# Kernel optimization log

Measured on AMD Instinct MI355X. Metric: run time of the kernel, lower is better.

## Reference

```python
import jax, jax.numpy as jnp
import numpy as np

B, M, N = 4, 2048, 2048
C, H, HD, L = 256, 4, 64, 9
THR = 0.1


def _rope(x, cos, sin):
    # x: (B,H,N,HD); cos/sin: (B,1,N,HD) with pair-interleaved values
    x1 = x[..., 0::2]
    x2 = x[..., 1::2]
    rot = jnp.stack([-x2, x1], axis=-1).reshape(x.shape)
    return x * cos + rot * sin


def _heads(x, b, n):
    return x.reshape(b, n, H, HD).transpose(0, 2, 1, 3)


def _merge(x, b, n):
    return x.transpose(0, 2, 1, 3).reshape(b, n, H * HD)


def _ffn(x, msg, W1, b1, g, beta, W2, b2):
    h = jnp.concatenate([x, msg], axis=-1) @ W1 + b1
    mu = h.mean(-1, keepdims=True)
    var = h.var(-1, keepdims=True)
    h = (h - mu) * jax.lax.rsqrt(var + 1e-5) * g + beta
    return jax.nn.gelu(h) @ W2 + b2


def _self_block(x, cos, sin, Wqkv, bqkv, Wo, bo, ff):
    b, n, _ = x.shape
    q, k, v = jnp.split(x @ Wqkv + bqkv, 3, axis=-1)
    q = _rope(_heads(q, b, n), cos, sin)
    k = _rope(_heads(k, b, n), cos, sin)
    v = _heads(v, b, n)
    attn = jax.nn.softmax(jnp.einsum('bhmd,bhnd->bhmn', q, k) / jnp.sqrt(jnp.float32(HD)), axis=-1)
    msg = _merge(jnp.einsum('bhmn,bhnd->bhmd', attn, v), b, n) @ Wo + bo
    return x + _ffn(x, msg, *ff)


def _cross_block(x0, x1, Wqk, bqk, Wv, bv, Wo, bo, ff):
    b, m, _ = x0.shape
    n = x1.shape[1]
    s = HD ** -0.25
    qk0 = _heads(x0 @ Wqk + bqk, b, m) * s
    qk1 = _heads(x1 @ Wqk + bqk, b, n) * s
    v0 = _heads(x0 @ Wv + bv, b, m)
    v1 = _heads(x1 @ Wv + bv, b, n)
    sim = jnp.einsum('bhmd,bhnd->bhmn', qk0, qk1)
    m0 = jnp.einsum('bhmn,bhnd->bhmd', jax.nn.softmax(sim, axis=3), v1)
    m1 = jnp.einsum('bhmn,bhmd->bhnd', jax.nn.softmax(sim, axis=2), v0)
    m0 = _merge(m0, b, m) @ Wo + bo
    m1 = _merge(m1, b, n) @ Wo + bo
    return x0 + _ffn(x0, m0, *ff), x1 + _ffn(x1, m1, *ff)


def _posenc(kpts, size, Wr):
    shift = size / 2.0
    scale = size.max() / 2.0
    knorm = (kpts - shift) / scale                      # (B,N,2)
    proj = knorm @ Wr                                   # (B,N,HD//2)
    cos = jnp.repeat(jnp.cos(proj), 2, axis=-1)[:, None, :, :]  # (B,1,N,HD)
    sin = jnp.repeat(jnp.sin(proj), 2, axis=-1)[:, None, :, :]
    return cos, sin


def setup_inputs() -> dict:
    key = jax.random.key(0)
    def nrm(i, shape, s=0.02):
        return (s * jax.random.normal(jax.random.fold_in(key, i), shape)).astype(jnp.float32)
    def uni(i, shape):
        return jax.random.uniform(jax.random.fold_in(key, i), shape, jnp.float32)
    wh = jnp.array([1024.0, 768.0], jnp.float32)
    return {
        'kpts0': uni(0, (B, M, 2)) * wh,
        'desc0': nrm(1, (B, M, C), 1.0),
        'kpts1': uni(2, (B, N, 2)) * wh,
        'desc1': nrm(3, (B, N, C), 1.0),
        'image_size': wh,
        'Wr': nrm(4, (2, HD // 2), 1.0),
        'saqkv_W': nrm(5, (L, C, 3 * C)),
        'saqkv_b': jnp.zeros((L, 3 * C), jnp.float32),
        'saout_W': nrm(6, (L, C, C)),
        'saout_b': jnp.zeros((L, C), jnp.float32),
        'saff_W1': nrm(7, (L, 2 * C, 2 * C)),
        'saff_b1': jnp.zeros((L, 2 * C), jnp.float32),
        'saff_g': jnp.ones((L, 2 * C), jnp.float32),
        'saff_beta': jnp.zeros((L, 2 * C), jnp.float32),
        'saff_W2': nrm(8, (L, 2 * C, C)),
        'saff_b2': jnp.zeros((L, C), jnp.float32),
        'caqk_W': nrm(9, (L, C, C)),
        'caqk_b': jnp.zeros((L, C), jnp.float32),
        'cav_W': nrm(10, (L, C, C)),
        'cav_b': jnp.zeros((L, C), jnp.float32),
        'caout_W': nrm(11, (L, C, C)),
        'caout_b': jnp.zeros((L, C), jnp.float32),
        'caff_W1': nrm(12, (L, 2 * C, 2 * C)),
        'caff_b1': jnp.zeros((L, 2 * C), jnp.float32),
        'caff_g': jnp.ones((L, 2 * C), jnp.float32),
        'caff_beta': jnp.zeros((L, 2 * C), jnp.float32),
        'caff_W2': nrm(13, (L, 2 * C, C)),
        'caff_b2': jnp.zeros((L, C), jnp.float32),
        'fproj_W': nrm(14, (C, C)),
        'fproj_b': jnp.zeros((C,), jnp.float32),
        'match_w': nrm(15, (C,)),
        'match_b': jnp.zeros((), jnp.float32),
    }


def reference(kpts0, desc0, kpts1, desc1, image_size, Wr,
              saqkv_W, saqkv_b, saout_W, saout_b,
              saff_W1, saff_b1, saff_g, saff_beta, saff_W2, saff_b2,
              caqk_W, caqk_b, cav_W, cav_b, caout_W, caout_b,
              caff_W1, caff_b1, caff_g, caff_beta, caff_W2, caff_b2,
              fproj_W, fproj_b, match_w, match_b):
    cos0, sin0 = _posenc(kpts0, image_size, Wr)
    cos1, sin1 = _posenc(kpts1, image_size, Wr)
    d0, d1 = desc0, desc1
    for i in range(L):
        ffs = (saff_W1[i], saff_b1[i], saff_g[i], saff_beta[i], saff_W2[i], saff_b2[i])
        d0 = _self_block(d0, cos0, sin0, saqkv_W[i], saqkv_b[i], saout_W[i], saout_b[i], ffs)
        d1 = _self_block(d1, cos1, sin1, saqkv_W[i], saqkv_b[i], saout_W[i], saout_b[i], ffs)
        ffc = (caff_W1[i], caff_b1[i], caff_g[i], caff_beta[i], caff_W2[i], caff_b2[i])
        d0, d1 = _cross_block(d0, d1, caqk_W[i], caqk_b[i], cav_W[i], cav_b[i], caout_W[i], caout_b[i], ffc)
    # sigmoid log-double-softmax assignment
    scale = C ** 0.25
    md0 = (d0 @ fproj_W + fproj_b) / scale
    md1 = (d1 @ fproj_W + fproj_b) / scale
    sim = jnp.einsum('bmd,bnd->bmn', md0, md1)
    z0 = d0 @ match_w + match_b                         # (B,M)
    z1 = d1 @ match_w + match_b                         # (B,N)
    inner = (jax.nn.log_softmax(sim, axis=2) + jax.nn.log_softmax(sim, axis=1)
             + jax.nn.log_sigmoid(z0)[:, :, None] + jax.nn.log_sigmoid(z1)[:, None, :])
    scores = jnp.zeros((B, M + 1, N + 1), sim.dtype)
    scores = scores.at[:, :M, :N].set(inner)
    scores = scores.at[:, :M, N].set(jax.nn.log_sigmoid(-z0))
    scores = scores.at[:, M, :N].set(jax.nn.log_sigmoid(-z1))
    # filter_matches: mutual nearest neighbor + threshold
    valid = scores[:, :-1, :-1]
    max0 = valid.max(axis=2)
    argmax0 = valid.argmax(axis=2)
    argmax1 = valid.argmax(axis=1)
    idx0 = jnp.arange(M)[None, :]
    idx1 = jnp.arange(N)[None, :]
    mutual0 = idx0 == jnp.take_along_axis(argmax1, argmax0, axis=1)
    mutual1 = idx1 == jnp.take_along_axis(argmax0, argmax1, axis=1)
    mscores0 = jnp.where(mutual0, jnp.exp(max0), 0.0)
    mscores1 = jnp.where(mutual1, jnp.take_along_axis(mscores0, argmax1, axis=1), 0.0)
    valid0 = mutual0 & (mscores0 > THR)
    valid1 = mutual1 & jnp.take_along_axis(valid0, argmax1, axis=1)
    m0 = jnp.where(valid0, argmax0, -1)
    m1 = jnp.where(valid1, argmax1, -1)
    return m0, m1, mscores0, mscores1, scores
```

## Files before the change

### kernel.cpp

```cpp
#include <hip/hip_runtime.h>
#include <hip/hip_bf16.h>
#include <cmath>

#define DEVI __device__ __forceinline__

constexpr int B_   = 4;
constexpr int M_   = 2048;
constexpr int C_   = 256;
constexpr int H_   = 4;
constexpr int HD_  = 64;
constexpr int L_   = 9;
constexpr int TOK_ = B_ * M_;
constexpr int C2_  = 2 * C_;
constexpr int C3_  = 3 * C_;
constexpr int NS_  = 2049;

typedef __attribute__((ext_vector_type(8))) short s16x8;
typedef __attribute__((ext_vector_type(4))) float f32x4;
typedef __attribute__((ext_vector_type(4))) unsigned short u16x4;

DEVI float logsig_f(float x) {
  if (x >= 0.0f) return -log1pf(__expf(-x));
  return x - log1pf(__expf(x));
}

DEVI float gelu_tanh(float x) {
  float x3 = x * x * x;
  float t = 0.7978845608028654f * (x + 0.044715f * x3);
  return x / (1.0f + __expf(-2.0f * t));
}

DEVI unsigned short f2bf(float x) {
  unsigned u = __float_as_uint(x);
  u += 0x7fffu + ((u >> 16) & 1u);
  return (unsigned short)(u >> 16);
}
DEVI float bf2f(unsigned short h) { return __uint_as_float((unsigned)h << 16); }

__global__ void posenc_kernel(const float* __restrict__ kpts, const float* __restrict__ wh,
                              const float* __restrict__ Wr, float* __restrict__ cc,
                              float* __restrict__ sc) {
  int idx = blockIdx.x * blockDim.x + threadIdx.x;
  if (idx >= B_ * M_ * 32) return;
  int j  = idx & 31;
  int bm = idx >> 5;
  float w = wh[0], h = wh[1];
  float smax = fmaxf(w, h) * 0.5f;
  float kx = (kpts[bm * 2 + 0] - w * 0.5f) / smax;
  float ky = (kpts[bm * 2 + 1] - h * 0.5f) / smax;
  float p = kx * Wr[j] + ky * Wr[32 + j];
  cc[bm * 32 + j] = cosf(p);
  sc[bm * 32 + j] = sinf(p);
}

__global__ void wconv_kernel(const float* __restrict__ W, unsigned short* __restrict__ Th,
                             unsigned short* __restrict__ Tl, int kbits, int N) {
  int idx = blockIdx.x * 256 + threadIdx.x;
  int k = idx & ((1 << kbits) - 1);
  int n = idx >> kbits;
  float x = W[(size_t)k * N + n];
  unsigned short h = f2bf(x);
  Th[idx] = h;
  Tl[idx] = f2bf(x - bf2f(h));
}

__global__ void wconv_layer_kernel(const float* __restrict__ qkv, const float* __restrict__ saout,
                                   const float* __restrict__ sw1, const float* __restrict__ sw2,
                                   const float* __restrict__ cqk, const float* __restrict__ cv,
                                   const float* __restrict__ cout_, const float* __restrict__ cw1,
                                   const float* __restrict__ cw2,
                                   unsigned short* __restrict__ Th, unsigned short* __restrict__ Tl) {
  int idx = blockIdx.x * 256 + threadIdx.x;
  const float* src; int kbits, N, rel;
  if      (idx <  196608) { src = qkv;   kbits = 8; N = 768; rel = idx; }
  else if (idx <  262144) { src = saout; kbits = 8; N = 256; rel = idx -  196608; }
  else if (idx <  524288) { src = sw1;   kbits = 9; N = 512; rel = idx -  262144; }
  else if (idx <  655360) { src = sw2;   kbits = 9; N = 256; rel = idx -  524288; }
  else if (idx <  720896) { src = cqk;   kbits = 8; N = 256; rel = idx -  655360; }
  else if (idx <  786432) { src = cv;    kbits = 8; N = 256; rel = idx -  720896; }
  else if (idx <  851968) { src = cout_; kbits = 8; N = 256; rel = idx -  786432; }
  else if (idx < 1114112) { src = cw1;   kbits = 9; N = 512; rel = idx -  851968; }
  else                    { src = cw2;   kbits = 9; N = 256; rel = idx - 1114112; }
  int k = rel & ((1 << kbits) - 1), n = rel >> kbits;
  float x = src[(size_t)k * N + n];
  unsigned short h = f2bf(x);
  Th[idx] = h;
  Tl[idx] = f2bf(x - bf2f(h));
}

__global__ void split_kernel(const float* __restrict__ src, unsigned short* __restrict__ h,
                             unsigned short* __restrict__ l) {
  int idx = blockIdx.x * 256 + threadIdx.x;
  float x = src[idx];
  unsigned short hb = f2bf(x);
  h[idx] = hb;
  l[idx] = f2bf(x - bf2f(hb));
}

__global__ __launch_bounds__(256) void prep_ropeqk_kernel(
    const float* __restrict__ S, const float* __restrict__ cc, const float* __restrict__ sc,
    unsigned short* __restrict__ Qh, unsigned short* __restrict__ Ql,
    unsigned short* __restrict__ Kh, unsigned short* __restrict__ Kl) {
  int idx = blockIdx.x * 256 + threadIdx.x;
  int j = idx & 31;
  int h = (idx >> 5) & 3;
  int tok = idx >> 7;
  int m = tok & 2047, b = tok >> 11;
  const float* row = S + (size_t)tok * 768 + h * 64 + 2 * j;
  float c = cc[(size_t)tok * 32 + j];
  float s = sc[(size_t)tok * 32 + j];
  float2 q = *(const float2*)row;
  float2 k = *(const float2*)(row + 256);
  float qx = q.x * c - q.y * s, qy = q.y * c + q.x * s;
  float kx = k.x * c - k.y * s, ky = k.y * c + k.x * s;
  size_t o = ((size_t)(b * 4 + h) * 2048 + m) * 64 + 2 * j;
  unsigned short q0 = f2bf(qx), q1 = f2bf(qy);
  ushort2 t;
  t.x = q0; t.y = q1;                       *(ushort2*)&Qh[o] = t;
  t.x = f2bf(qx - bf2f(q0)); t.y = f2bf(qy - bf2f(q1)); *(ushort2*)&Ql[o] = t;
  unsigned short k0 = f2bf(kx), k1 = f2bf(ky);
  t.x = k0; t.y = k1;                       *(ushort2*)&Kh[o] = t;
  t.x = f2bf(kx - bf2f(k0)); t.y = f2bf(ky - bf2f(k1)); *(ushort2*)&Kl[o] = t;
}

__global__ __launch_bounds__(256) void prep_vt_kernel(
    const float* __restrict__ S, int ld, int vcol,
    unsigned short* __restrict__ Vth, unsigned short* __restrict__ Vtl) {
  int idx = blockIdx.x * 256 + threadIdx.x;
  int mq = idx & 511; int m0 = mq << 2;
  int d = (idx >> 9) & 63;
  int bh = idx >> 15;
  int b = bh >> 2, h = bh & 3;
  const float* base = S + ((size_t)(b * 2048) + m0) * ld + vcol + h * 64 + d;
  u16x4 hv, lv;
#pragma unroll
  for (int i = 0; i < 4; i++) {
    float x = base[(size_t)i * ld];
    unsigned short hb = f2bf(x);
    hv[i] = hb;
    lv[i] = f2bf(x - bf2f(hb));
  }
  size_t o = ((size_t)bh * 64 + d) * 2048 + m0;
  *(u16x4*)&Vth[o] = hv;
  *(u16x4*)&Vtl[o] = lv;
}

__global__ __launch_bounds__(256, 3) void mgemm_kernel(
    const unsigned short* __restrict__ A1h, const unsigned short* __restrict__ A1l,
    const unsigned short* __restrict__ A2h, const unsigned short* __restrict__ A2l,
    int lda, int kSplit,
    const unsigned short* __restrict__ WTh, const unsigned short* __restrict__ WTl,
    const float* __restrict__ bias, const float* __restrict__ res,
    float* __restrict__ outf, int ldo,
    unsigned short* __restrict__ outh, unsigned short* __restrict__ outl, int nsplit,
    unsigned short* __restrict__ tvh, unsigned short* __restrict__ tvl,
    int K, float oscale) {
  __shared__ alignas(16) unsigned short Ash[128 * 64];
  __shared__ alignas(16) unsigned short Asl[128 * 64];
  __shared__ alignas(16) unsigned short Bsh[64 * 64];
  __shared__ alignas(16) unsigned short Bsl[64 * 64];
  int tid = threadIdx.x;
  int rowBase = blockIdx.y << 7;
  int colBase = blockIdx.x << 6;
  int lr = tid & 15, lg = (tid >> 4) & 3;
  int wid = tid >> 6, wm = wid >> 1, wn = wid & 1;
  int sw = (lr & 7) << 3;
  f32x4 acc[4][2] = {};

  for (int k0 = 0; k0 < K; k0 += 64) {
    const unsigned short *Ah, *Al;
    int kloc;
    if (k0 < kSplit) { Ah = A1h; Al = A1l; kloc = k0; }
    else             { Ah = A2h; Al = A2l; kloc = k0 - kSplit; }
    __syncthreads();
#pragma unroll
    for (int i = 0; i < 8; i++) {
      int idx = tid + (i << 8);
      int r = idx >> 4;
      int kc = (idx & 15) << 2;
      size_t g = (size_t)(rowBase + r) * lda + kloc + kc;
      u16x4 hv = *(const u16x4*)&Ah[g];
      u16x4 lv = *(const u16x4*)&Al[g];
      int col = kc ^ ((r & 7) << 3);
      *(u16x4*)&Ash[r * 64 + col] = hv;
      *(u16x4*)&Asl[r * 64 + col] = lv;
    }
#pragma unroll
    for (int i = 0; i < 4; i++) {
      int idx = tid + (i << 8);
      int rn = idx >> 4;
      int kc = (idx & 15) << 2;
      size_t g = (size_t)(colBase + rn) * K + k0 + kc;
      u16x4 hv = *(const u16x4*)&WTh[g];
      u16x4 lv = *(const u16x4*)&WTl[g];
      int col = kc ^ ((rn & 7) << 3);
      *(u16x4*)&Bsh[rn * 64 + col] = hv;
      *(u16x4*)&Bsl[rn * 64 + col] = lv;
    }
    __syncthreads();
#pragma unroll
    for (int c = 0; c < 2; c++) {
      int kcol = (c << 5) + (lg << 3);
      s16x8 ah[4], al[4], bh[2], bl[2];
#pragma unroll
      for (int mi = 0; mi < 4; mi++) {
        int off = (wm * 64 + mi * 16 + lr) * 64 + (kcol ^ sw);
        ah[mi] = *(const s16x8*)&Ash[off];
        al[mi] = *(const s16x8*)&Asl[off];
      }
#pragma unroll
      for (int ni = 0; ni < 2; ni++) {
        int off = (wn * 32 + ni * 16 + lr) * 64 + (kcol ^ sw);
        bh[ni] = *(const s16x8*)&Bsh[off];
        bl[ni] = *(const s16x8*)&Bsl[off];
      }
#pragma unroll
      for (int mi = 0; mi < 4; mi++)
#pragma unroll
        for (int ni = 0; ni < 2; ni++) {
          f32x4 t = acc[mi][ni];
          t = __builtin_amdgcn_mfma_f32_16x16x32_bf16(ah[mi], bl[ni], t, 0, 0, 0);
          t = __builtin_amdgcn_mfma_f32_16x16x32_bf16(al[mi], bh[ni], t, 0, 0, 0);
          t = __builtin_amdgcn_mfma_f32_16x16x32_bf16(ah[mi], bh[ni], t, 0, 0, 0);
          acc[mi][ni] = t;
        }
    }
  }
#pragma unroll
  for (int mi = 0; mi < 4; mi++) {
    int row0 = rowBase + wm * 64 + mi * 16 + lg * 4;
#pragma unroll
    for (int ni = 0; ni < 2; ni++) {
      int col = colBase + wn * 32 + ni * 16 + lr;
      float bc = bias ? bias[col] : 0.0f;
      float vj[4];
      size_t of0 = (size_t)row0 * ldo + col;
#pragma unroll
      for (int j = 0; j < 4; j++) {
        float v = (acc[mi][ni][j] + bc) * oscale;
        if (res) v += res[of0 + (size_t)j * ldo];
        vj[j] = v;
      }
      if (outf) {
#pragma unroll
        for (int j = 0; j < 4; j++) outf[of0 + (size_t)j * ldo] = vj[j];
      }
      bool plain = outh && (col < nsplit);
      if (plain) {
        size_t o0 = (size_t)row0 * 256 + col;
#pragma unroll
        for (int j = 0; j < 4; j++) {
          unsigned short hb = f2bf(vj[j]);
          outh[o0 + (size_t)j * 256] = hb;
          outl[o0 + (size_t)j * 256] = f2bf(vj[j] - bf2f(hb));
        }
      } else if (tvh) {
        int cc2 = outh ? (col - nsplit) : col;
        int hh = cc2 >> 6, d = cc2 & 63;
        int bb = row0 >> 11, m0 = row0 & 2047;
        u16x4 hv, lv;
#pragma unroll
        for (int j = 0; j < 4; j++) {
          unsigned short hb = f2bf(vj[j]);
          hv[j] = hb;
          lv[j] = f2bf(vj[j] - bf2f(hb));
        }
        size_t tvo = ((size_t)(bb * 4 + hh) * 64 + d) * 2048 + m0;
        *(u16x4*)&tvh[tvo] = hv;
        *(u16x4*)&tvl[tvo] = lv;
      }
    }
  }
}

__global__ __launch_bounds__(256, 2) void flashm2_kernel(
    const unsigned short* __restrict__ Qh, const unsigned short* __restrict__ Ql, int ldq, int hq,
    const unsigned short* __restrict__ Kh, const unsigned short* __restrict__ Kl, int ldk, int hk,
    const unsigned short* __restrict__ Vth, const unsigned short* __restrict__ Vtl,
    unsigned short* __restrict__ Oh, unsigned short* __restrict__ Ol, float scale) {
  __shared__ alignas(16) unsigned short Ksh[64 * 64];
  __shared__ alignas(16) unsigned short Ksl[64 * 64];
  __shared__ alignas(16) unsigned short Vsh[64 * 64];
  __shared__ alignas(16) unsigned short Vsl[64 * 64];
  __shared__ alignas(16) unsigned short Ph[64 * 64];
  __shared__ alignas(16) unsigned short Pl[64 * 64];
  int bh = blockIdx.y;
  int b = bh >> 2, h = bh & 3;
  int mBase = blockIdx.x * 64;
  size_t qbase = (size_t)b * (M_ * C_) + (size_t)h * hq;
  size_t kbase = (size_t)b * (M_ * C_) + (size_t)h * hk;
  size_t vbase = (size_t)bh * (64 * 2048);
  int tid = threadIdx.x;
  int lane = tid & 63, w = tid >> 6;
  int lr = lane & 15, lg = lane >> 4;

  s16x8 qh[2], ql[2];
  {
    int m = mBase + w * 16 + lr;
#pragma unroll
    for (int c = 0; c < 2; c++) {
      size_t g = qbase + (size_t)m * ldq + c * 32 + lg * 8;
      qh[c] = *(const s16x8*)&Qh[g];
      ql[c] = *(const s16x8*)&Ql[g];
    }
  }

  float m_run[4], l_run[4];
  f32x4 oacc[4];
#pragma unroll
  for (int j = 0; j < 4; j++) { m_run[j] = -INFINITY; l_run[j] = 0.0f; }
#pragma unroll
  for (int g = 0; g < 4; g++) oacc[g] = (f32x4){0.f, 0.f, 0.f, 0.f};

  for (int t0 = 0; t0 < M_; t0 += 64) {
    __syncthreads();
#pragma unroll
    for (int i = 0; i < 4; i++) {
      int idx = tid + (i << 8);
      int key = idx >> 4;
      int d0 = (idx & 15) << 2;
      size_t g = kbase + (size_t)(t0 + key) * ldk + d0;
      int cswz = d0 ^ ((key & 7) << 3);
      *(u16x4*)&Ksh[key * 64 + cswz] = *(const u16x4*)&Kh[g];
      *(u16x4*)&Ksl[key * 64 + cswz] = *(const u16x4*)&Kl[g];
      int d = idx >> 4;
      int kc = (idx & 15) << 2;
      size_t gv = vbase + (size_t)d * 2048 + t0 + kc;
      int kk = kc ^ (((d ^ (d >> 2)) & 7) << 3);
      *(u16x4*)&Vsh[d * 64 + kk] = *(const u16x4*)&Vth[gv];
      *(u16x4*)&Vsl[d * 64 + kk] = *(const u16x4*)&Vtl[gv];
    }
    __syncthreads();

    f32x4 sacc[4];
#pragma unroll
    for (int f = 0; f < 4; f++) sacc[f] = (f32x4){0.f, 0.f, 0.f, 0.f};
#pragma unroll
    for (int f = 0; f < 4; f++) {
#pragma unroll
      for (int c = 0; c < 2; c++) {
        int key = f * 16 + lr;
        int kb = c * 32 + lg * 8;
        int off = key * 64 + (kb ^ ((key & 7) << 3));
        s16x8 kh = *(const s16x8*)&Ksh[off];
        s16x8 kl = *(const s16x8*)&Ksl[off];
        f32x4 t = sacc[f];
        t = __builtin_amdgcn_mfma_f32_16x16x32_bf16(qh[c], kl, t, 0, 0, 0);
        t = __builtin_amdgcn_mfma_f32_16x16x32_bf16(ql[c], kh, t, 0, 0, 0);
        t = __builtin_amdgcn_mfma_f32_16x16x32_bf16(qh[c], kh, t, 0, 0, 0);
        sacc[f] = t;
      }
    }
#pragma unroll
    for (int f = 0; f < 4; f++)
#pragma unroll
      for (int j = 0; j < 4; j++) sacc[f][j] *= scale;

    float mnew[4], alpha[4], lsum[4];
#pragma unroll
    for (int j = 0; j < 4; j++) {
      float v = fmaxf(fmaxf(sacc[0][j], sacc[1][j]), fmaxf(sacc[2][j], sacc[3][j]));
      v = fmaxf(v, __shfl_xor(v, 1));
      v = fmaxf(v, __shfl_xor(v, 2));
      v = fmaxf(v, __shfl_xor(v, 4));
      v = fmaxf(v, __shfl_xor(v, 8));
      mnew[j] = fmaxf(m_run[j], v);
      alpha[j] = __expf(m_run[j] - mnew[j]);
      lsum[j] = 0.0f;
    }
#pragma unroll
    for (int f = 0; f < 4; f++) {
#pragma unroll
      for (int j = 0; j < 4; j++) {
        float p = __expf(sacc[f][j] - mnew[j]);
// ... 194 lines not shown
  if (lane == 0) { max_out[row] = best; am_out[row] = bi; }
}

__global__ void colamax1_kernel(const float* __restrict__ sco, float* __restrict__ pv,
                                int* __restrict__ pi) {
  int col = blockIdx.x * 256 + threadIdx.x;
  int rc = blockIdx.y, b = blockIdx.z;
  const float* base = sco + (size_t)b * NS_ * NS_ + col;
  float best = -INFINITY; int bi = 0;
  for (int r = rc * 256; r < rc * 256 + 256; r++) {
    float v = base[(size_t)r * NS_];
    if (v > best) { best = v; bi = r; }
  }
  size_t o = ((size_t)b * 8 + rc) * 2048 + col;
  pv[o] = best; pi[o] = bi;
}

__global__ void colamax2_kernel(const float* __restrict__ pv, const int* __restrict__ pi,
                                int* __restrict__ am1) {
  int i = blockIdx.x * 256 + threadIdx.x;
  int b = i >> 11, col = i & 2047;
  float best = -INFINITY; int bi = 0;
  for (int rc = 0; rc < 8; rc++) {
    size_t o = ((size_t)b * 8 + rc) * 2048 + col;
    float v = pv[o];
    if (v > best) { best = v; bi = pi[o]; }
  }
  am1[i] = bi;
}

__global__ void edge_kernel(const float* __restrict__ lsn0, const float* __restrict__ lsn1,
                            float* __restrict__ sco) {
  int i = blockIdx.x * blockDim.x + threadIdx.x;
  if (i >= B_ * M_) return;
  int b = i >> 11, t = i & 2047;
  sco[((size_t)b * NS_ + t) * NS_ + 2048] = lsn0[i];
  sco[((size_t)b * NS_ + 2048) * NS_ + t] = lsn1[i];
  if (t == 0) sco[((size_t)b * NS_ + 2048) * NS_ + 2048] = 0.0f;
}

__global__ void match0ws_kernel(const int* __restrict__ am0, const int* __restrict__ am1,
                                const float* __restrict__ max0, float* __restrict__ ms0f,
                                int* __restrict__ val0) {
  int i = blockIdx.x * blockDim.x + threadIdx.x;
  if (i >= B_ * M_) return;
  int b = i >> 11, m = i & 2047;
  int a0 = am0[i];
  bool mutual = (am1[b * M_ + a0] == m);
  float ms = mutual ? __expf(max0[i]) : 0.0f;
  ms0f[i] = ms;
  val0[i] = (mutual && ms > 0.1f) ? 1 : 0;
}

__global__ void finalout_kernel(const int* __restrict__ am0, const int* __restrict__ am1,
                                const float* __restrict__ ms0f, const int* __restrict__ val0,
                                float* __restrict__ out) {
  int i = blockIdx.x * blockDim.x + threadIdx.x;
  if (i >= B_ * M_) return;
  int b = i >> 11, t = i & 2047;
  int a0 = am0[i];
  bool mut0 = (am1[b * M_ + a0] == t);
  float ms0 = ms0f[i];
  bool v0 = mut0 && (ms0 > 0.1f);
  out[i] = v0 ? (float)a0 : -1.0f;
  out[2 * B_ * M_ + i] = ms0;
  int a1 = am1[i];
  bool mut1 = (am0[b * M_ + a1] == t);
  float ms1 = mut1 ? ms0f[b * M_ + a1] : 0.0f;
  bool v1 = mut1 && (val0[b * M_ + a1] != 0);
  out[B_ * M_ + i] = v1 ? (float)a1 : -1.0f;
  out[3 * B_ * M_ + i] = ms1;
}

constexpr size_t WOFF_QKV   = 0;
constexpr size_t WOFF_SAOUT = 196608;
constexpr size_t WOFF_SAW1  = 262144;
constexpr size_t WOFF_SAW2  = 524288;
constexpr size_t WOFF_CAQK  = 655360;
constexpr size_t WOFF_CAOUT = 786432;
constexpr size_t WOFF_CAW1  = 851968;
constexpr size_t WOFF_CAW2  = 1114112;
constexpr size_t WELEMS_    = 1245184;

constexpr size_t PLN   = (size_t)TOK_ * C_;
constexpr size_t OXS0  = 2 * WELEMS_;
constexpr size_t OXS1  = OXS0 + 2 * PLN;
constexpr size_t OBA   = OXS1 + 2 * PLN;
constexpr size_t OBB   = OBA + 2 * PLN;
constexpr size_t OBC   = OBB + 2 * PLN;
constexpr size_t OBD   = OBC + 2 * PLN;
constexpr size_t OBE   = OBD + 2 * PLN;

extern "C" void kernel_launch(void* const* d_in, const int* in_sizes, int n_in,
                              void* d_out, int out_size, void* d_ws, size_t ws_size,
                              hipStream_t stream) {
  const float* kpts0      = (const float*)d_in[0];
  const float* desc0      = (const float*)d_in[1];
  const float* kpts1      = (const float*)d_in[2];
  const float* desc1      = (const float*)d_in[3];
  const float* image_size = (const float*)d_in[4];
  const float* Wr         = (const float*)d_in[5];
  const float* saqkv_W    = (const float*)d_in[6];
  const float* saqkv_b    = (const float*)d_in[7];
  const float* saout_W    = (const float*)d_in[8];
  const float* saout_b    = (const float*)d_in[9];
  const float* saff_W1    = (const float*)d_in[10];
  const float* saff_b1    = (const float*)d_in[11];
  const float* saff_g     = (const float*)d_in[12];
  const float* saff_beta  = (const float*)d_in[13];
  const float* saff_W2    = (const float*)d_in[14];
  const float* saff_b2    = (const float*)d_in[15];
  const float* caqk_W     = (const float*)d_in[16];
  const float* caqk_b     = (const float*)d_in[17];
  const float* cav_W      = (const float*)d_in[18];
  const float* cav_b      = (const float*)d_in[19];
  const float* caout_W    = (const float*)d_in[20];
  const float* caout_b    = (const float*)d_in[21];
  const float* caff_W1    = (const float*)d_in[22];
  const float* caff_b1    = (const float*)d_in[23];
  const float* caff_g     = (const float*)d_in[24];
  const float* caff_beta  = (const float*)d_in[25];
  const float* caff_W2    = (const float*)d_in[26];
  const float* caff_b2    = (const float*)d_in[27];
  const float* fproj_W    = (const float*)d_in[28];
  const float* fproj_b    = (const float*)d_in[29];
  const float* match_w    = (const float*)d_in[30];
  const float* match_b    = (const float*)d_in[31];

  float* ofp = (float*)d_out;
  float* SCO = ofp + 4 * B_ * M_;
  unsigned short* SCu = (unsigned short*)SCO;

  constexpr size_t N = (size_t)TOK_ * C_;
  constexpr size_t Qc = (size_t)B_ * M_ * 32;
  float* Wp  = (float*)d_ws;
  float* D0  = Wp;
  float* D1  = D0 + N;
  float* CC0 = D1 + N;
  float* SC0 = CC0 + Qc;
  float* CC1 = SC0 + Qc;
  float* SC1 = CC1 + Qc;
  float* S0  = SC1 + Qc;
  float* S1  = S0 + N;
  float* S2  = S1 + N;
  float* S3  = S2 + N;
  float* S4  = S3 + N;
  (void)S4;

  unsigned short* WTH = SCu;
  unsigned short* WTL = SCu + WELEMS_;

  float* LS0  = S2;
  float* LSN0 = LS0 + 8192;
  float* LS1  = LSN0 + 8192;
  float* LSN1 = LS1 + 8192;
  float* RT   = LSN1 + 8192;
  float* CT   = RT + 8192;
  float* MAX0 = CT + 8192;
  float* MS0F = MAX0 + 8192;
  int*   AM0  = (int*)(MS0F + 8192);
  int*   AM1  = AM0 + 8192;
  int*   VAL0 = AM1 + 8192;
  float* CB   = (float*)(VAL0 + 8192);
  float* PM = S3;
  float* PL = PM + 65536;
  float* PV = PL + 65536;
  int*   PI = (int*)(PV + 65536);
  unsigned short* MD0u = (unsigned short*)S0;
  unsigned short* MD1u = (unsigned short*)S1;

  auto Hp = [&](size_t off) { return SCu + off; };
  auto Lp = [&](size_t off) { return SCu + off + PLN; };

  auto mgemm = [&](const unsigned short* a1h, const unsigned short* a1l,
                   const unsigned short* a2h, const unsigned short* a2l,
                   int lda, int kSplit, const unsigned short* wth, const unsigned short* wtl,
                   const float* bias, const float* res, float* outf, int ldo,
                   unsigned short* outh, unsigned short* outl, int nsplit,
                   unsigned short* tvh, unsigned short* tvl,
                   int K, int Ncols, int Mrows, float osc) {
    mgemm_kernel<<<dim3(Ncols >> 6, Mrows >> 7), 256, 0, stream>>>(
        a1h, a1l, a2h, a2l, lda, kSplit, wth, wtl,
        bias, res, outf, ldo, outh, outl, nsplit, tvh, tvl, K, osc);
  };

  auto ffn = [&](float* X, unsigned short* xsh, unsigned short* xsl,
                 unsigned short* msgh, unsigned short* msgl,
                 size_t offW1, const float* b1, const float* g, const float* be,
                 size_t offW2, const float* b2) {
    mgemm(xsh, xsl, msgh, msgl, C_, C_, WTH + offW1, WTL + offW1,
          b1, nullptr, S0, C2_, nullptr, nullptr, 0, nullptr, nullptr, C2_, C2_, TOK_, 1.0f);
    ln_gelu_kernel<<<TOK_, 256, 0, stream>>>(S0, g, be, Hp(OBC), Hp(OBD));
    mgemm(Hp(OBC), Hp(OBD), Hp(OBC), Hp(OBD), C2_, C2_, WTH + offW2, WTL + offW2,
          b2, X, X, C_, xsh, xsl, C_, nullptr, nullptr, C2_, C_, TOK_, 1.0f);
  };

  auto self_block = [&](float* X, unsigned short* xsh, unsigned short* xsl,
                        const float* cc, const float* sc, int l) {
    const float* bqkv = saqkv_b + (size_t)l * C3_;
    const float* bo   = saout_b + (size_t)l * C_;
    mgemm(xsh, xsl, xsh, xsl, C_, C_, WTH + WOFF_QKV, WTL + WOFF_QKV,
          bqkv, nullptr, S0, C3_, nullptr, nullptr, 0, nullptr, nullptr, C_, C3_, TOK_, 1.0f);
    prep_ropeqk_kernel<<<4096, 256, 0, stream>>>(S0, cc, sc, Hp(OBA), Lp(OBA), Hp(OBB), Lp(OBB));
    prep_vt_kernel<<<2048, 256, 0, stream>>>(S0, C3_, C2_, Hp(OBC), Lp(OBC));
    flashm2_kernel<<<dim3(M_ / 64, B_ * H_), 256, 0, stream>>>(
        Hp(OBA), Lp(OBA), 64, 2048 * 64, Hp(OBB), Lp(OBB), 64, 2048 * 64,
        Hp(OBC), Lp(OBC), Hp(OBE), Lp(OBE), 0.125f);
    mgemm(Hp(OBE), Lp(OBE), Hp(OBE), Lp(OBE), C_, C_, WTH + WOFF_SAOUT, WTL + WOFF_SAOUT,
          bo, nullptr, nullptr, C_, Hp(OBA), Lp(OBA), C_, nullptr, nullptr, C_, C_, TOK_, 1.0f);
    ffn(X, xsh, xsl, Hp(OBA), Lp(OBA),
        WOFF_SAW1, saff_b1 + (size_t)l * C2_,
        saff_g + (size_t)l * C2_, saff_beta + (size_t)l * C2_,
        WOFF_SAW2, saff_b2 + (size_t)l * C_);
  };

  auto cross_block = [&](int l) {
    const float* bo  = caout_b + (size_t)l * C_;
    const float* b1  = caff_b1 + (size_t)l * C2_;
    const float* g   = caff_g + (size_t)l * C2_;
    const float* be  = caff_beta + (size_t)l * C2_;
    const float* b2  = caff_b2 + (size_t)l * C_;
    hipMemcpyAsync(CB, caqk_b + (size_t)l * C_, C_ * sizeof(float),
                   hipMemcpyDeviceToDevice, stream);
    hipMemcpyAsync(CB + C_, cav_b + (size_t)l * C_, C_ * sizeof(float),
                   hipMemcpyDeviceToDevice, stream);
    mgemm(Hp(OXS0), Lp(OXS0), Hp(OXS0), Lp(OXS0), C_, C_, WTH + WOFF_CAQK, WTL + WOFF_CAQK,
          CB, nullptr, nullptr, C_, Hp(OBA), Lp(OBA), C_, Hp(OBC), Lp(OBC), C_, C2_, TOK_, 1.0f);
    mgemm(Hp(OXS1), Lp(OXS1), Hp(OXS1), Lp(OXS1), C_, C_, WTH + WOFF_CAQK, WTL + WOFF_CAQK,
          CB, nullptr, nullptr, C_, Hp(OBB), Lp(OBB), C_, Hp(OBD), Lp(OBD), C_, C2_, TOK_, 1.0f);
    flashm2_kernel<<<dim3(M_ / 64, B_ * H_), 256, 0, stream>>>(
        Hp(OBA), Lp(OBA), C_, 64, Hp(OBB), Lp(OBB), C_, 64,
        Hp(OBD), Lp(OBD), Hp(OBE), Lp(OBE), 0.125f);
    flashm2_kernel<<<dim3(M_ / 64, B_ * H_), 256, 0, stream>>>(
        Hp(OBB), Lp(OBB), C_, 64, Hp(OBA), Lp(OBA), C_, 64,
        Hp(OBC), Lp(OBC), Hp(OBD), Lp(OBD), 0.125f);
    mgemm(Hp(OBE), Lp(OBE), Hp(OBE), Lp(OBE), C_, C_, WTH + WOFF_CAOUT, WTL + WOFF_CAOUT,
          bo, nullptr, nullptr, C_, Hp(OBA), Lp(OBA), C_, nullptr, nullptr, C_, C_, TOK_, 1.0f);
    mgemm(Hp(OBD), Lp(OBD), Hp(OBD), Lp(OBD), C_, C_, WTH + WOFF_CAOUT, WTL + WOFF_CAOUT,
          bo, nullptr, nullptr, C_, Hp(OBB), Lp(OBB), C_, nullptr, nullptr, C_, C_, TOK_, 1.0f);
    ffn(D0, Hp(OXS0), Lp(OXS0), Hp(OBA), Lp(OBA), WOFF_CAW1, b1, g, be, WOFF_CAW2, b2);
    ffn(D1, Hp(OXS1), Lp(OXS1), Hp(OBB), Lp(OBB), WOFF_CAW1, b1, g, be, WOFF_CAW2, b2);
  };

  hipMemcpyAsync(D0, desc0, N * sizeof(float), hipMemcpyDeviceToDevice, stream);
  hipMemcpyAsync(D1, desc1, N * sizeof(float), hipMemcpyDeviceToDevice, stream);
  split_kernel<<<PLN / 256, 256, 0, stream>>>(desc0, Hp(OXS0), Lp(OXS0));
  split_kernel<<<PLN / 256, 256, 0, stream>>>(desc1, Hp(OXS1), Lp(OXS1));
  posenc_kernel<<<(B_ * M_ * 32 + 255) / 256, 256, 0, stream>>>(kpts0, image_size, Wr, CC0, SC0);
  posenc_kernel<<<(B_ * M_ * 32 + 255) / 256, 256, 0, stream>>>(kpts1, image_size, Wr, CC1, SC1);

  for (int l = 0; l < L_; l++) {
    wconv_layer_kernel<<<WELEMS_ / 256, 256, 0, stream>>>(
        saqkv_W + (size_t)l * C_ * C3_, saout_W + (size_t)l * C_ * C_,
        saff_W1 + (size_t)l * C2_ * C2_, saff_W2 + (size_t)l * C2_ * C_,
        caqk_W + (size_t)l * C_ * C_, cav_W + (size_t)l * C_ * C_,
        caout_W + (size_t)l * C_ * C_, caff_W1 + (size_t)l * C2_ * C2_,
        caff_W2 + (size_t)l * C2_ * C_, WTH, WTL);
    self_block(D0, Hp(OXS0), Lp(OXS0), CC0, SC0, l);
    self_block(D1, Hp(OXS1), Lp(OXS1), CC1, SC1, l);
    cross_block(l);
  }

  wconv_kernel<<<(C_ << 8) >> 8, 256, 0, stream>>>(fproj_W, WTH, WTL, 8, C_);
  mgemm(Hp(OXS0), Lp(OXS0), Hp(OXS0), Lp(OXS0), C_, C_, WTH, WTL,
        fproj_b, nullptr, nullptr, C_, MD0u, MD0u + PLN, C_, nullptr, nullptr,
        C_, C_, TOK_, 0.25f);
  mgemm(Hp(OXS1), Lp(OXS1), Hp(OXS1), Lp(OXS1), C_, C_, WTH, WTL,
        fproj_b, nullptr, nullptr, C_, MD1u, MD1u + PLN, C_, nullptr, nullptr,
        C_, C_, TOK_, 0.25f);
  z_kernel<<<2048, 256, 0, stream>>>(D0, match_w, match_b, LS0, LSN0);
  z_kernel<<<2048, 256, 0, stream>>>(D1, match_w, match_b, LS1, LSN1);
  for (int b = 0; b < B_; b++) {
    size_t ao = (size_t)b * M_ * C_;
    mgemm(MD0u + ao, MD0u + PLN + ao, MD0u + ao, MD0u + PLN + ao, C_, C_,
          MD1u + ao, MD1u + PLN + ao, nullptr, nullptr,
          SCO + (size_t)b * NS_ * NS_, NS_, nullptr, nullptr, 0, nullptr, nullptr,
          C_, M_, M_, 2.0f);
  }
  edge_kernel<<<32, 256, 0, stream>>>(LSN0, LSN1, SCO);
  lse_row_kernel<<<2048, 256, 0, stream>>>(SCO, LS0, RT);
  colred1_kernel<<<dim3(8, 8, 4), 256, 0, stream>>>(SCO, PM, PL);
  colred2_kernel<<<32, 256, 0, stream>>>(PM, PL, LS1, CT);
  upd_rowargmax_kernel<<<2048, 256, 0, stream>>>(RT, CT, SCO, MAX0, AM0);
  colamax1_kernel<<<dim3(8, 8, 4), 256, 0, stream>>>(SCO, PV, PI);
  colamax2_kernel<<<32, 256, 0, stream>>>(PV, PI, AM1);
  match0ws_kernel<<<32, 256, 0, stream>>>(AM0, AM1, MAX0, MS0F, VAL0);
  finalout_kernel<<<32, 256, 0, stream>>>(AM0, AM1, MS0F, VAL0, ofp);

  (void)in_sizes; (void)n_in; (void)out_size; (void)ws_size;
}
```

Measured before the change: 7.933 ms.

## Fuse RoPE/V-transpose into QKV GEMM epilogue and batch both images per launch

Moves the RoPE rotation and the bf16 hi/lo split of Q/K, plus the transposed V write, into the QKV GEMM epilogue, using a lane shuffle to fetch the paired element. This removes the fp32 QKV round trip and two prep kernels. It also lays out both images' activations contiguously so the out-projections, FFNs, cross QK/V projection and final projection each run as one launch over 2x tokens. Cross-attention biases are packed once up front instead of by per-layer memcpys. The cost is a more complex GEMM epilogue with scattered 2-byte stores and a reworked buffer-aliasing scheme that has to stay correct.

```diff
diff --git a/kernel.cpp b/kernel.cpp
--- a/kernel.cpp
+++ b/kernel.cpp
@@ -88,6 +88,14 @@
   Tl[idx] = f2bf(x - bf2f(h));
 }
 
+__global__ void cbias_kernel(const float* __restrict__ qkb, const float* __restrict__ vb,
+                             float* __restrict__ cb) {
+  int i = blockIdx.x * 256 + threadIdx.x;
+  if (i >= L_ * 512) return;
+  int l = i >> 9, c = i & 511;
+  cb[i] = (c < 256) ? qkb[l * 256 + c] : vb[l * 256 + (c - 256)];
+}
+
 __global__ void split_kernel(const float* __restrict__ src, unsigned short* __restrict__ h,
                              unsigned short* __restrict__ l) {
   int idx = blockIdx.x * 256 + threadIdx.x;
@@ -95,54 +103,6 @@
   unsigned short hb = f2bf(x);
   h[idx] = hb;
   l[idx] = f2bf(x - bf2f(hb));
-}
-
-__global__ __launch_bounds__(256) void prep_ropeqk_kernel(
-    const float* __restrict__ S, const float* __restrict__ cc, const float* __restrict__ sc,
-    unsigned short* __restrict__ Qh, unsigned short* __restrict__ Ql,
-    unsigned short* __restrict__ Kh, unsigned short* __restrict__ Kl) {
-  int idx = blockIdx.x * 256 + threadIdx.x;
-  int j = idx & 31;
-  int h = (idx >> 5) & 3;
-  int tok = idx >> 7;
-  int m = tok & 2047, b = tok >> 11;
-  const float* row = S + (size_t)tok * 768 + h * 64 + 2 * j;
-  float c = cc[(size_t)tok * 32 + j];
-  float s = sc[(size_t)tok * 32 + j];
-  float2 q = *(const float2*)row;
-  float2 k = *(const float2*)(row + 256);
-  float qx = q.x * c - q.y * s, qy = q.y * c + q.x * s;
-  float kx = k.x * c - k.y * s, ky = k.y * c + k.x * s;
-  size_t o = ((size_t)(b * 4 + h) * 2048 + m) * 64 + 2 * j;
-  unsigned short q0 = f2bf(qx), q1 = f2bf(qy);
-  ushort2 t;
-  t.x = q0; t.y = q1;                       *(ushort2*)&Qh[o] = t;
-  t.x = f2bf(qx - bf2f(q0)); t.y = f2bf(qy - bf2f(q1)); *(ushort2*)&Ql[o] = t;
-  unsigned short k0 = f2bf(kx), k1 = f2bf(ky);
-  t.x = k0; t.y = k1;                       *(ushort2*)&Kh[o] = t;
-  t.x = f2bf(kx - bf2f(k0)); t.y = f2bf(ky - bf2f(k1)); *(ushort2*)&Kl[o] = t;
-}
-
-__global__ __launch_bounds__(256) void prep_vt_kernel(
-    const float* __restrict__ S, int ld, int vcol,
-    unsigned short* __restrict__ Vth, unsigned short* __restrict__ Vtl) {
-  int idx = blockIdx.x * 256 + threadIdx.x;
-  int mq = idx & 511; int m0 = mq << 2;
-  int d = (idx >> 9) & 63;
-  int bh = idx >> 15;
-  int b = bh >> 2, h = bh & 3;
-  const float* base = S + ((size_t)(b * 2048) + m0) * ld + vcol + h * 64 + d;
-  u16x4 hv, lv;
-#pragma unroll
-  for (int i = 0; i < 4; i++) {
-    float x = base[(size_t)i * ld];
-    unsigned short hb = f2bf(x);
-    hv[i] = hb;
-    lv[i] = f2bf(x - bf2f(hb));
-  }
-  size_t o = ((size_t)bh * 64 + d) * 2048 + m0;
-  *(u16x4*)&Vth[o] = hv;
-  *(u16x4*)&Vtl[o] = lv;
 }
 
 __global__ __launch_bounds__(256, 3) void mgemm_kernel(
@@ -154,6 +114,9 @@
     float* __restrict__ outf, int ldo,
     unsigned short* __restrict__ outh, unsigned short* __restrict__ outl, int nsplit,
     unsigned short* __restrict__ tvh, unsigned short* __restrict__ tvl,
+    const float* __restrict__ ccp, const float* __restrict__ scp,
+    unsigned short* __restrict__ qph, unsigned short* __restrict__ qpl,
+    unsigned short* __restrict__ kph, unsigned short* __restrict__ kpl,
     int K, float oscale) {
   __shared__ alignas(16) unsigned short Ash[128 * 64];
   __shared__ alignas(16) unsigned short Asl[128 * 64];
@@ -241,33 +204,73 @@
         if (res) v += res[of0 + (size_t)j * ldo];
         vj[j] = v;
       }
-      if (outf) {
-#pragma unroll
-        for (int j = 0; j < 4; j++) outf[of0 + (size_t)j * ldo] = vj[j];
-      }
-      bool plain = outh && (col < nsplit);
-      if (plain) {
-        size_t o0 = (size_t)row0 * 256 + col;
-#pragma unroll
-        for (int j = 0; j < 4; j++) {
-          unsigned short hb = f2bf(vj[j]);
-          outh[o0 + (size_t)j * 256] = hb;
-          outl[o0 + (size_t)j * 256] = f2bf(vj[j] - bf2f(hb));
+      if (ccp) {
+        if (col < 512) {
+          float pv[4];
+#pragma unroll
+          for (int j = 0; j < 4; j++) pv[j] = __shfl_xor(vj[j], 1);
+          int d = col & 63;
+          int hh = (col >> 6) & 3;
+          int ji = (d >> 1) & 31;
+          bool isK = col >= 256;
+          unsigned short* dh = isK ? kph : qph;
+          unsigned short* dl = isK ? kpl : qpl;
+          int bb = row0 >> 11;
+#pragma unroll
+          for (int j = 0; j < 4; j++) {
+            int tok = row0 + j;
+            float c = ccp[(size_t)tok * 32 + ji];
+            float s = scp[(size_t)tok * 32 + ji];
+            float r = (col & 1) ? (vj[j] * c + pv[j] * s)
+                                : (vj[j] * c - pv[j] * s);
+            size_t o = ((size_t)(bb * 4 + hh) * 2048 + (tok & 2047)) * 64 + d;
+            unsigned short hb = f2bf(r);
+            dh[o] = hb;
+            dl[o] = f2bf(r - bf2f(hb));
+          }
+        } else {
+          int cc2 = col - 512;
+          int hh = cc2 >> 6, d = cc2 & 63;
+          int bb = row0 >> 11, mv = row0 & 2047;
+          u16x4 hv, lv;
+#pragma unroll
+          for (int j = 0; j < 4; j++) {
+            unsigned short hb = f2bf(vj[j]);
+            hv[j] = hb; lv[j] = f2bf(vj[j] - bf2f(hb));
+          }
+          size_t tvo = ((size_t)(bb * 4 + hh) * 64 + d) * 2048 + mv;
+          *(u16x4*)&tvh[tvo] = hv;
+          *(u16x4*)&tvl[tvo] = lv;
         }
-      } else if (tvh) {
-        int cc2 = outh ? (col - nsplit) : col;
-        int hh = cc2 >> 6, d = cc2 & 63;
-        int bb = row0 >> 11, m0 = row0 & 2047;
-        u16x4 hv, lv;
-#pragma unroll
-        for (int j = 0; j < 4; j++) {
-          unsigned short hb = f2bf(vj[j]);
-          hv[j] = hb;
-          lv[j] = f2bf(vj[j] - bf2f(hb));
+      } else {
+        if (outf) {
+#pragma unroll
+          for (int j = 0; j < 4; j++) outf[of0 + (size_t)j * ldo] = vj[j];
         }
-        size_t tvo = ((size_t)(bb * 4 + hh) * 64 + d) * 2048 + m0;
-        *(u16x4*)&tvh[tvo] = hv;
-        *(u16x4*)&tvl[tvo] = lv;
+        bool plain = outh && (col < nsplit);
+        if (plain) {
+          size_t o0 = (size_t)row0 * 256 + col;
+#pragma unroll
+          for (int j = 0; j < 4; j++) {
+            unsigned short hb = f2bf(vj[j]);
+            outh[o0 + (size_t)j * 256] = hb;
+            outl[o0 + (size_t)j * 256] = f2bf(vj[j] - bf2f(hb));
+          }
+        } else if (tvh) {
+          int cc2 = outh ? (col - nsplit) : col;
+          int hh = cc2 >> 6, d = cc2 & 63;
+          int bb = row0 >> 11, mv = row0 & 2047;
+          u16x4 hv, lv;
+#pragma unroll
+          for (int j = 0; j < 4; j++) {
+            unsigned short hb = f2bf(vj[j]);
+            hv[j] = hb;
+            lv[j] = f2bf(vj[j] - bf2f(hb));
+          }
+          size_t tvo = ((size_t)(bb * 4 + hh) * 64 + d) * 2048 + mv;
+          *(u16x4*)&tvh[tvo] = hv;
+          *(u16x4*)&tvl[tvo] = lv;
+        }
       }
     }
   }
@@ -276,7 +279,7 @@
 __global__ __launch_bounds__(256, 2) void flashm2_kernel(
     const unsigned short* __restrict__ Qh, const unsigned short* __restrict__ Ql, int ldq, int hq,
     const unsigned short* __restrict__ Kh, const unsigned short* __restrict__ Kl, int ldk, int hk,
-    const unsigned short* __restrict__ Vth, const unsigned short* __restrict__ Vtl,
+    const unsigned short* __restrict__ Vth, const unsigned short* __restrict__ Vtl, int voff,
     unsigned short* __restrict__ Oh, unsigned short* __restrict__ Ol, float scale) {
   __shared__ alignas(16) unsigned short Ksh[64 * 64];
   __shared__ alignas(16) unsigned short Ksl[64 * 64];
@@ -289,7 +292,7 @@
   int mBase = blockIdx.x * 64;
   size_t qbase = (size_t)b * (M_ * C_) + (size_t)h * hq;
   size_t kbase = (size_t)b * (M_ * C_) + (size_t)h * hk;
-  size_t vbase = (size_t)bh * (64 * 2048);
+  size_t vbase = (size_t)(voff + bh) * (64 * 2048);
   int tid = threadIdx.x;
   int lane = tid & 63, w = tid >> 6;
   int lr = lane & 15, lg = lane >> 4;
@@ -650,14 +653,10 @@
 constexpr size_t WOFF_CAW2  = 1114112;
 constexpr size_t WELEMS_    = 1245184;
 
-constexpr size_t PLN   = (size_t)TOK_ * C_;
-constexpr size_t OXS0  = 2 * WELEMS_;
-constexpr size_t OXS1  = OXS0 + 2 * PLN;
-constexpr size_t OBA   = OXS1 + 2 * PLN;
-constexpr size_t OBB   = OBA + 2 * PLN;
-constexpr size_t OBC   = OBB + 2 * PLN;
-constexpr size_t OBD   = OBC + 2 * PLN;
-constexpr size_t OBE   = OBD + 2 * PLN;
+constexpr size_t PLN  = (size_t)TOK_ * C_;
+constexpr size_t XHO  = 2 * WELEMS_;
+constexpr size_t XLO  = XHO + 2 * PLN;
+constexpr size_t POOL = XLO + 2 * PLN;
 
 extern "C" void kernel_launch(void* const* d_in, const int* in_sizes, int n_in,
                               void* d_out, int out_size, void* d_ws, size_t ws_size,
@@ -713,10 +712,12 @@
   float* S2  = S1 + N;
   float* S3  = S2 + N;
   float* S4  = S3 + N;
-  (void)S4;
 
   unsigned short* WTH = SCu;
   unsigned short* WTL = SCu + WELEMS_;
+  unsigned short* XH  = SCu + XHO;
+  unsigned short* XL  = SCu + XLO;
+  auto Pu = [&](int k) { return SCu + POOL + (size_t)k * PLN; };
 
   float* LS0  = S2;
   float* LSN0 = LS0 + 8192;
@@ -729,93 +730,46 @@
   int*   AM0  = (int*)(MS0F + 8192);
   int*   AM1  = AM0 + 8192;
   int*   VAL0 = AM1 + 8192;
-  float* CB   = (float*)(VAL0 + 8192);
   float* PM = S3;
   float* PL = PM + 65536;
   float* PV = PL + 65536;
   int*   PI = (int*)(PV + 65536);
-  unsigned short* MD0u = (unsigned short*)S0;
-  unsigned short* MD1u = (unsigned short*)S1;
-
-  auto Hp = [&](size_t off) { return SCu + off; };
-  auto Lp = [&](size_t off) { return SCu + off + PLN; };
-
-  auto mgemm = [&](const unsigned short* a1h, const unsigned short* a1l,
-                   const unsigned short* a2h, const unsigned short* a2l,
-                   int lda, int kSplit, const unsigned short* wth, const unsigned short* wtl,
-                   const float* bias, const float* res, float* outf, int ldo,
-                   unsigned short* outh, unsigned short* outl, int nsplit,
-                   unsigned short* tvh, unsigned short* tvl,
-                   int K, int Ncols, int Mrows, float osc) {
+  float* CB = S4;
+  unsigned short* MDu = (unsigned short*)S0;
+
+  auto mg = [&](const unsigned short* a1h, const unsigned short* a1l,
+                const unsigned short* a2h, const unsigned short* a2l,
+                int lda, int kSplit, const unsigned short* wth, const unsigned short* wtl,
+                const float* bias, const float* res, float* outf, int ldo,
+                unsigned short* outh, unsigned short* outl, int nsplit,
+                unsigned short* tvh, unsigned short* tvl,
+                const float* ccp, const float* scp,
+                unsigned short* qph, unsigned short* qpl,
+                unsigned short* kph, unsigned short* kpl,
+                int K, int Ncols, int Mrows, float osc) {
     mgemm_kernel<<<dim3(Ncols >> 6, Mrows >> 7), 256, 0, stream>>>(
-        a1h, a1l, a2h, a2l, lda, kSplit, wth, wtl,
-        bias, res, outf, ldo, outh, outl, nsplit, tvh, tvl, K, osc);
+        a1h, a1l, a2h, a2l, lda, kSplit, wth, wtl, bias, res, outf, ldo,
+        outh, outl, nsplit, tvh, tvl, ccp, scp, qph, qpl, kph, kpl, K, osc);
   };
 
-  auto ffn = [&](float* X, unsigned short* xsh, unsigned short* xsl,
-                 unsigned short* msgh, unsigned short* msgl,
-                 size_t offW1, const float* b1, const float* g, const float* be,
-                 size_t offW2, const float* b2) {
-    mgemm(xsh, xsl, msgh, msgl, C_, C_, WTH + offW1, WTL + offW1,
-          b1, nullptr, S0, C2_, nullptr, nullptr, 0, nullptr, nullptr, C2_, C2_, TOK_, 1.0f);
-    ln_gelu_kernel<<<TOK_, 256, 0, stream>>>(S0, g, be, Hp(OBC), Hp(OBD));
-    mgemm(Hp(OBC), Hp(OBD), Hp(OBC), Hp(OBD), C2_, C2_, WTH + offW2, WTL + offW2,
-          b2, X, X, C_, xsh, xsl, C_, nullptr, nullptr, C2_, C_, TOK_, 1.0f);
-  };
-
-  auto self_block = [&](float* X, unsigned short* xsh, unsigned short* xsl,
-                        const float* cc, const float* sc, int l) {
-    const float* bqkv = saqkv_b + (size_t)l * C3_;
-    const float* bo   = saout_b + (size_t)l * C_;
-    mgemm(xsh, xsl, xsh, xsl, C_, C_, WTH + WOFF_QKV, WTL + WOFF_QKV,
-          bqkv, nullptr, S0, C3_, nullptr, nullptr, 0, nullptr, nullptr, C_, C3_, TOK_, 1.0f);
-    prep_ropeqk_kernel<<<4096, 256, 0, stream>>>(S0, cc, sc, Hp(OBA), Lp(OBA), Hp(OBB), Lp(OBB));
-    prep_vt_kernel<<<2048, 256, 0, stream>>>(S0, C3_, C2_, Hp(OBC), Lp(OBC));
-    flashm2_kernel<<<dim3(M_ / 64, B_ * H_), 256, 0, stream>>>(
-        Hp(OBA), Lp(OBA), 64, 2048 * 64, Hp(OBB), Lp(OBB), 64, 2048 * 64,
-        Hp(OBC), Lp(OBC), Hp(OBE), Lp(OBE), 0.125f);
-    mgemm(Hp(OBE), Lp(OBE), Hp(OBE), Lp(OBE), C_, C_, WTH + WOFF_SAOUT, WTL + WOFF_SAOUT,
-          bo, nullptr, nullptr, C_, Hp(OBA), Lp(OBA), C_, nullptr, nullptr, C_, C_, TOK_, 1.0f);
-    ffn(X, xsh, xsl, Hp(OBA), Lp(OBA),
-        WOFF_SAW1, saff_b1 + (size_t)l * C2_,
-        saff_g + (size_t)l * C2_, saff_beta + (size_t)l * C2_,
-        WOFF_SAW2, saff_b2 + (size_t)l * C_);
-  };
-
-  auto cross_block = [&](int l) {
-    const float* bo  = caout_b + (size_t)l * C_;
-    const float* b1  = caff_b1 + (size_t)l * C2_;
-    const float* g   = caff_g + (size_t)l * C2_;
-    const float* be  = caff_beta + (size_t)l * C2_;
-    const float* b2  = caff_b2 + (size_t)l * C_;
-    hipMemcpyAsync(CB, caqk_b + (size_t)l * C_, C_ * sizeof(float),
-                   hipMemcpyDeviceToDevice, stream);
-    hipMemcpyAsync(CB + C_, cav_b + (size_t)l * C_, C_ * sizeof(float),
-                   hipMemcpyDeviceToDevice, stream);
-    mgemm(Hp(OXS0), Lp(OXS0), Hp(OXS0), Lp(OXS0), C_, C_, WTH + WOFF_CAQK, WTL + WOFF_CAQK,
-          CB, nullptr, nullptr, C_, Hp(OBA), Lp(OBA), C_, Hp(OBC), Lp(OBC), C_, C2_, TOK_, 1.0f);
-    mgemm(Hp(OXS1), Lp(OXS1), Hp(OXS1), Lp(OXS1), C_, C_, WTH + WOFF_CAQK, WTL + WOFF_CAQK,
-          CB, nullptr, nullptr, C_, Hp(OBB), Lp(OBB), C_, Hp(OBD), Lp(OBD), C_, C2_, TOK_, 1.0f);
-    flashm2_kernel<<<dim3(M_ / 64, B_ * H_), 256, 0, stream>>>(
-        Hp(OBA), Lp(OBA), C_, 64, Hp(OBB), Lp(OBB), C_, 64,
-        Hp(OBD), Lp(OBD), Hp(OBE), Lp(OBE), 0.125f);
-    flashm2_kernel<<<dim3(M_ / 64, B_ * H_), 256, 0, stream>>>(
-        Hp(OBB), Lp(OBB), C_, 64, Hp(OBA), Lp(OBA), C_, 64,
-        Hp(OBC), Lp(OBC), Hp(OBD), Lp(OBD), 0.125f);
-    mgemm(Hp(OBE), Lp(OBE), Hp(OBE), Lp(OBE), C_, C_, WTH + WOFF_CAOUT, WTL + WOFF_CAOUT,
-          bo, nullptr, nullptr, C_, Hp(OBA), Lp(OBA), C_, nullptr, nullptr, C_, C_, TOK_, 1.0f);
-    mgemm(Hp(OBD), Lp(OBD), Hp(OBD), Lp(OBD), C_, C_, WTH + WOFF_CAOUT, WTL + WOFF_CAOUT,
-          bo, nullptr, nullptr, C_, Hp(OBB), Lp(OBB), C_, nullptr, nullptr, C_, C_, TOK_, 1.0f);
-    ffn(D0, Hp(OXS0), Lp(OXS0), Hp(OBA), Lp(OBA), WOFF_CAW1, b1, g, be, WOFF_CAW2, b2);
-    ffn(D1, Hp(OXS1), Lp(OXS1), Hp(OBB), Lp(OBB), WOFF_CAW1, b1, g, be, WOFF_CAW2, b2);
+  auto ffn2 = [&](size_t offW1, const float* b1, const float* g, const float* be,
+                  size_t offW2, const float* b2) {
+    mg(XH, XL, Pu(0), Pu(2), C_, C_, WTH + offW1, WTL + offW1,
+       b1, nullptr, S0, C2_, nullptr, nullptr, 0, nullptr, nullptr,
+       nullptr, nullptr, nullptr, nullptr, nullptr, nullptr, C2_, C2_, 2 * TOK_, 1.0f);
+    ln_gelu_kernel<<<2 * TOK_, 256, 0, stream>>>(S0, g, be, Pu(0), Pu(4));
+    mg(Pu(0), Pu(4), Pu(0), Pu(4), C2_, C2_, WTH + offW2, WTL + offW2,
+       b2, D0, D0, C_, XH, XL, C_, nullptr, nullptr,
+       nullptr, nullptr, nullptr, nullptr, nullptr, nullptr, C2_, C_, 2 * TOK_, 1.0f);
   };
 
   hipMemcpyAsync(D0, desc0, N * sizeof(float), hipMemcpyDeviceToDevice, stream);
   hipMemcpyAsync(D1, desc1, N * sizeof(float), hipMemcpyDeviceToDevice, stream);
-  split_kernel<<<PLN / 256, 256, 0, stream>>>(desc0, Hp(OXS0), Lp(OXS0));
-  split_kernel<<<PLN / 256, 256, 0, stream>>>(desc1, Hp(OXS1), Lp(OXS1));
+  split_kernel<<<PLN / 256, 256, 0, stream>>>(desc0, XH, XL);
+  split_kernel<<<PLN / 256, 256, 0, stream>>>(desc1, XH + PLN, XL + PLN);
   posenc_kernel<<<(B_ * M_ * 32 + 255) / 256, 256, 0, stream>>>(kpts0, image_size, Wr, CC0, SC0);
   posenc_kernel<<<(B_ * M_ * 32 + 255) / 256, 256, 0, stream>>>(kpts1, image_size, Wr, CC1, SC1);
+  cbias_kernel<<<(L_ * 512 + 255) / 256, 256, 0, stream>>>(caqk_b, cav_b, CB);
 
   for (int l = 0; l < L_; l++) {
     wconv_layer_kernel<<<WELEMS_ / 256, 256, 0, stream>>>(
@@ -824,26 +778,61 @@
         caqk_W + (size_t)l * C_ * C_, cav_W + (size_t)l * C_ * C_,
         caout_W + (size_t)l * C_ * C_, caff_W1 + (size_t)l * C2_ * C2_,
         caff_W2 + (size_t)l * C2_ * C_, WTH, WTL);
-    self_block(D0, Hp(OXS0), Lp(OXS0), CC0, SC0, l);
-    self_block(D1, Hp(OXS1), Lp(OXS1), CC1, SC1, l);
-    cross_block(l);
+    const float* bqkv = saqkv_b + (size_t)l * C3_;
+    const float* bo   = saout_b + (size_t)l * C_;
+
+    for (int i = 0; i < 2; i++) {
+      const float* cc = i ? CC1 : CC0;
+      const float* sc = i ? SC1 : SC0;
+      mg(XH + i * PLN, XL + i * PLN, XH + i * PLN, XL + i * PLN, C_, C_,
+         WTH + WOFF_QKV, WTL + WOFF_QKV, bqkv, nullptr, nullptr, C3_,
+         nullptr, nullptr, 0, Pu(4), Pu(5),
+         cc, sc, Pu(0), Pu(1), Pu(2), Pu(3), C_, C3_, TOK_, 1.0f);
+      flashm2_kernel<<<dim3(M_ / 64, B_ * H_), 256, 0, stream>>>(
+          Pu(0), Pu(1), 64, 2048 * 64, Pu(2), Pu(3), 64, 2048 * 64,
+          Pu(4), Pu(5), 0, Pu(6 + i), Pu(8 + i), 0.125f);
+    }
+    mg(Pu(6), Pu(8), Pu(6), Pu(8), C_, C_, WTH + WOFF_SAOUT, WTL + WOFF_SAOUT,
+       bo, nullptr, nullptr, C_, Pu(0), Pu(2), C_, nullptr, nullptr,
+       nullptr, nullptr, nullptr, nullptr, nullptr, nullptr, C_, C_, 2 * TOK_, 1.0f);
+    ffn2(WOFF_SAW1, saff_b1 + (size_t)l * C2_,
+         saff_g + (size_t)l * C2_, saff_beta + (size_t)l * C2_,
+         WOFF_SAW2, saff_b2 + (size_t)l * C_);
+
+    mg(XH, XL, XH, XL, C_, C_, WTH + WOFF_CAQK, WTL + WOFF_CAQK,
+       CB + (size_t)l * 512, nullptr, nullptr, C2_, Pu(0), Pu(2), C_, Pu(4), Pu(6),
+       nullptr, nullptr, nullptr, nullptr, nullptr, nullptr, C_, C2_, 2 * TOK_, 1.0f);
+    flashm2_kernel<<<dim3(M_ / 64, B_ * H_), 256, 0, stream>>>(
+        Pu(0), Pu(2), C_, 64, Pu(1), Pu(3), C_, 64,
+        Pu(4), Pu(6), 16, Pu(8), Pu(9), 0.125f);
+    flashm2_kernel<<<dim3(M_ / 64, B_ * H_), 256, 0, stream>>>(
+        Pu(1), Pu(3), C_, 64, Pu(0), Pu(2), C_, 64,
+        Pu(4), Pu(6), 0, Pu(5), Pu(7), 0.125f);
+    mg(Pu(8), Pu(9), Pu(8), Pu(9), C_, C_, WTH + WOFF_CAOUT, WTL + WOFF_CAOUT,
+       caout_b + (size_t)l * C_, nullptr, nullptr, C_, Pu(0), Pu(2), C_,
+       nullptr, nullptr, nullptr, nullptr, nullptr, nullptr, nullptr, nullptr,
+       C_, C_, TOK_, 1.0f);
+    mg(Pu(5), Pu(7), Pu(5), Pu(7), C_, C_, WTH + WOFF_CAOUT, WTL + WOFF_CAOUT,
+       caout_b + (size_t)l * C_, nullptr, nullptr, C_, Pu(1), Pu(3), C_,
+       nullptr, nullptr, nullptr, nullptr, nullptr, nullptr, nullptr, nullptr,
+       C_, C_, TOK_, 1.0f);
+    ffn2(WOFF_CAW1, caff_b1 + (size_t)l * C2_,
+         caff_g + (size_t)l * C2_, caff_beta + (size_t)l * C2_,
+         WOFF_CAW2, caff_b2 + (size_t)l * C_);
   }
 
   wconv_kernel<<<(C_ << 8) >> 8, 256, 0, stream>>>(fproj_W, WTH, WTL, 8, C_);
-  mgemm(Hp(OXS0), Lp(OXS0), Hp(OXS0), Lp(OXS0), C_, C_, WTH, WTL,
-        fproj_b, nullptr, nullptr, C_, MD0u, MD0u + PLN, C_, nullptr, nullptr,
-        C_, C_, TOK_, 0.25f);
-  mgemm(Hp(OXS1), Lp(OXS1), Hp(OXS1), Lp(OXS1), C_, C_, WTH, WTL,
-        fproj_b, nullptr, nullptr, C_, MD1u, MD1u + PLN, C_, nullptr, nullptr,
-        C_, C_, TOK_, 0.25f);
+  mg(XH, XL, XH, XL, C_, C_, WTH, WTL, fproj_b, nullptr, nullptr, C_,
+     MDu, MDu + 2 * PLN, C_, nullptr, nullptr,
+     nullptr, nullptr, nullptr, nullptr, nullptr, nullptr, C_, C_, 2 * TOK_, 0.25f);
   z_kernel<<<2048, 256, 0, stream>>>(D0, match_w, match_b, LS0, LSN0);
   z_kernel<<<2048, 256, 0, stream>>>(D1, match_w, match_b, LS1, LSN1);
   for (int b = 0; b < B_; b++) {
     size_t ao = (size_t)b * M_ * C_;
-    mgemm(MD0u + ao, MD0u + PLN + ao, MD0u + ao, MD0u + PLN + ao, C_, C_,
-          MD1u + ao, MD1u + PLN + ao, nullptr, nullptr,
-          SCO + (size_t)b * NS_ * NS_, NS_, nullptr, nullptr, 0, nullptr, nullptr,
-          C_, M_, M_, 2.0f);
+    mg(MDu + ao, MDu + 2 * PLN + ao, MDu + ao, MDu + 2 * PLN + ao, C_, C_,
+       MDu + PLN + ao, MDu + 3 * PLN + ao, nullptr, nullptr,
+       SCO + (size_t)b * NS_ * NS_, NS_, nullptr, nullptr, 0, nullptr, nullptr,
+       nullptr, nullptr, nullptr, nullptr, nullptr, nullptr, C_, M_, M_, 2.0f);
   }
   edge_kernel<<<32, 256, 0, stream>>>(LSN0, LSN1, SCO);
   lse_row_kernel<<<2048, 256, 0, stream>>>(SCO, LS0, RT);
```

Result: faster. 7.158 ms (-9.8%).
